# Kernel optimization log

Hardware: AMD Instinct MI355X
Metric: run time of the kernel (lower is better)

Reference implementation:

```python
import jax, jax.numpy as jnp
import numpy as np

B, L, H, NH, P = 4, 1024, 1024, 16, 2048
HD = H // NH


def setup_inputs() -> dict:
    key = jax.random.key(0)
    ks = jax.random.split(key, 6)
    x = jax.random.normal(ks[0], (B, L, H), dtype=jnp.float32)
    # torch.nn.Linear weights are [out, in]
    Wqkv = jax.random.normal(ks[1], (3 * H, H), dtype=jnp.float32) * 0.02
    bqkv = jnp.zeros((3 * H,), dtype=jnp.float32)
    Wo = jax.random.normal(ks[2], (H, H), dtype=jnp.float32) * 0.02
    bo = jnp.zeros((H,), dtype=jnp.float32)
    Er = jax.random.normal(ks[3], (NH, P, HD), dtype=jnp.float32)
    # causal mask: True where attention is disallowed (masked_fill semantics)
    mask = jnp.triu(jnp.ones((L, L), dtype=bool), k=1)
    return {"x": x, "mask": mask, "Wqkv": Wqkv, "bqkv": bqkv,
            "Wo": Wo, "bo": bo, "Er": Er}


def reference(x, mask, Wqkv, bqkv, Wo, bo, Er):
    b, l, d = x.shape
    nh, p, hd = Er.shape
    qkv = x @ Wqkv.T + bqkv                      # [b, l, 3d]
    q, k, v = jnp.split(qkv, 3, axis=-1)
    q = q.reshape(b, l, nh, hd).transpose(0, 2, 1, 3)   # [b, nh, l, hd]
    k = k.reshape(b, l, nh, hd).transpose(0, 2, 1, 3)
    v = v.reshape(b, l, nh, hd).transpose(0, 2, 1, 3)

    scores = jnp.einsum('bnlh,bnkh->bnlk', q, k) / jnp.sqrt(
        jnp.asarray(hd, dtype=x.dtype))

    # relative positions (j - i), torch negative-index wraparound -> mod p
    pos = jnp.arange(l)
    rel = (pos[None, :] - pos[:, None]) % p      # [l, l] in [0, p)
    # Equivalent to einsum('bnlh,rnlkh->bnlk', q, Er[:, rel][None]) but
    # computed as q @ Er^T over all positions then gathered (same math,
    # avoids materializing the [nh, l, l, hd] tensor).
    QEr_full = jnp.einsum('bnlh,nph->bnlp', q, Er)       # [b, nh, l, p]
    i_idx = pos[:, None]                          # broadcasts with rel
    QEr = QEr_full[:, :, i_idx, rel]              # [b, nh, l, l]

    a = scores + QEr
    a = jnp.where(mask, -jnp.inf, a)
    a = jax.nn.softmax(a, axis=-1)                # dropout: eval mode (identity)

    out = jnp.einsum('bnlk,bnkh->bnlh', a, v)     # [b, nh, l, hd]
    out = out.transpose(0, 2, 1, 3).reshape(b, l, d)
    return out @ Wo.T + bo
```

## Files before the change

### kernel.cpp

```cpp
#include <hip/hip_runtime.h>

typedef unsigned short u16;
typedef __bf16 bf16x8 __attribute__((ext_vector_type(8)));
typedef unsigned short u16x8 __attribute__((ext_vector_type(8)));
typedef float f32x4 __attribute__((ext_vector_type(4)));

#define MFMA16(a, b, c) __builtin_amdgcn_mfma_f32_16x16x32_bf16((a), (b), (c), 0, 0, 0)

#define WAVE_LDS_FENCE() do { \
  asm volatile("s_waitcnt lgkmcnt(0)" ::: "memory"); \
  __builtin_amdgcn_sched_barrier(0); \
} while (0)

#define GLDS(gp, lp) __builtin_amdgcn_global_load_lds( \
    (const __attribute__((address_space(1))) unsigned int*)(gp), \
    (__attribute__((address_space(3))) unsigned int*)(lp), 16, 0, 0)

__device__ __forceinline__ u16 f2b(float f) {
  unsigned u = __float_as_uint(f);
  u += 0x7fffu + ((u >> 16) & 1u);
  return (u16)(u >> 16);
}
__device__ __forceinline__ float b2f(u16 h) {
  return __uint_as_float(((unsigned)h) << 16);
}

__global__ void cvt_bf16(const float* __restrict__ src, u16* __restrict__ dst, int n4) {
  int i = blockIdx.x * blockDim.x + threadIdx.x;
  if (i >= n4) return;
  float4 v = *(const float4*)(src + (size_t)i * 4);
  *(ushort4*)(dst + (size_t)i * 4) = make_ushort4(f2b(v.x), f2b(v.y), f2b(v.z), f2b(v.w));
}

__global__ void build_F(const float* __restrict__ Er, u16* __restrict__ Fb) {
  int i = blockIdx.x * blockDim.x + threadIdx.x;
  int base = i * 4;
  int d = base & 63;
  int m = (base >> 6) & 1023;
  int n = base >> 16;
  int sm = (2048 - m) & 2047;
  float4 v = *(const float4*)(Er + ((size_t)(n * 2048 + sm) * 64 + d));
  *(ushort4*)(Fb + (size_t)base) = make_ushort4(f2b(v.x), f2b(v.y), f2b(v.z), f2b(v.w));
}

__global__ __launch_bounds__(256) void transpose_v(const u16* __restrict__ V, u16* __restrict__ Vt) {
  __shared__ u16 T[4096];
  const int bn = blockIdx.x, i0 = blockIdx.y * 64;
  const int t = threadIdx.x;
#pragma unroll
  for (int s = 0; s < 2; ++s) {
    int ch = t + 256 * s;
    int i = ch >> 3, c = ch & 7;
    u16x8 v = *(const u16x8*)&V[(size_t)((bn << 10) + i0 + i) * 64 + c * 8];
#pragma unroll
    for (int e = 0; e < 8; ++e) {
      int d = c * 8 + e;
      T[d * 64 + ((((i >> 3) ^ (d & 7) ^ ((d >> 3) & 7)) & 7) << 3) + (i & 7)] = v[e];
    }
  }
  __syncthreads();
#pragma unroll
  for (int s = 0; s < 2; ++s) {
    int ch = t + 256 * s;
    int d = ch >> 3, cc = ch & 7;
    u16x8 o = *(const u16x8*)&T[d * 64 + (((cc ^ (d & 7) ^ ((d >> 3) & 7)) & 7) << 3)];
    *(u16x8*)&Vt[(size_t)((bn << 6) + d) * 1024 + i0 + cc * 8] = o;
  }
}

__global__ __launch_bounds__(256) void gemm_qkv(const u16* __restrict__ A, const u16* __restrict__ Bw,
                                                const float* __restrict__ bias,
                                                u16* __restrict__ Qo, u16* __restrict__ Ko,
                                                u16* __restrict__ Vo) {
  __shared__ u16 As[8][128][8];
  __shared__ u16 Bs[8][128][8];
  const int m0 = blockIdx.y * 128, n0 = blockIdx.x * 128;
  const int t = threadIdx.x, lane = t & 63, w = t >> 6;
  const int wr = w >> 1, wc = w & 1;
  const int l16 = lane & 15, lg = lane >> 4;
  f32x4 acc[4][4] = {};

  for (int k0 = 0; k0 < 1024; k0 += 64) {
#pragma unroll
    for (int s = 0; s < 4; ++s) {
      int c = t + 256 * s;
      int r = c & 127, g = c >> 7;
      GLDS(&A[(size_t)(m0 + r) * 1024 + k0 + g * 8], &As[g][r][0]);
      GLDS(&Bw[(size_t)(n0 + r) * 1024 + k0 + g * 8], &Bs[g][r][0]);
    }
    __syncthreads();
#pragma unroll
    for (int kk = 0; kk < 2; ++kk) {
      bf16x8 af[4], bfr[4];
#pragma unroll
      for (int m = 0; m < 4; ++m) af[m] = *(const bf16x8*)&As[lg + 4 * kk][wr * 64 + m * 16 + l16][0];
#pragma unroll
      for (int n = 0; n < 4; ++n) bfr[n] = *(const bf16x8*)&Bs[lg + 4 * kk][wc * 64 + n * 16 + l16][0];
#pragma unroll
      for (int m = 0; m < 4; ++m)
#pragma unroll
        for (int n = 0; n < 4; ++n) acc[m][n] = MFMA16(af[m], bfr[n], acc[m][n]);
    }
    __syncthreads();
  }

#pragma unroll
  for (int n = 0; n < 4; ++n) {
    int col = n0 + wc * 64 + n * 16 + l16;
    float bq = bias[col];
    int which = col >> 10;
    int h = col & 1023;
    int head = h >> 6, d = h & 63;
    u16* dst = which == 0 ? Qo : (which == 1 ? Ko : Vo);
    float scale = which == 1 ? 0.125f : 1.0f;
#pragma unroll
    for (int m = 0; m < 4; ++m) {
#pragma unroll
      for (int r = 0; r < 4; ++r) {
        int row = m0 + wr * 64 + m * 16 + lg * 4 + r;
        int b = row >> 10, ii = row & 1023;
        float v = (acc[m][n][r] + bq) * scale;
        dst[(size_t)(((b * 16 + head) << 10) + ii) * 64 + d] = f2b(v);
      }
    }
  }
}

__global__ __launch_bounds__(256) void gemm_out(const u16* __restrict__ A, const u16* __restrict__ Bw,
                                                const float* __restrict__ bias, float* __restrict__ Co) {
  __shared__ u16 As[8][128][8];
  __shared__ u16 Bs[8][128][8];
  const int m0 = blockIdx.y * 128, n0 = blockIdx.x * 128;
  const int t = threadIdx.x, lane = t & 63, w = t >> 6;
  const int wr = w >> 1, wc = w & 1;
  const int l16 = lane & 15, lg = lane >> 4;
  f32x4 acc[4][4] = {};

  for (int k0 = 0; k0 < 1024; k0 += 64) {
#pragma unroll
    for (int s = 0; s < 4; ++s) {
      int c = t + 256 * s;
      int r = c & 127, g = c >> 7;
      GLDS(&A[(size_t)(m0 + r) * 1024 + k0 + g * 8], &As[g][r][0]);
      GLDS(&Bw[(size_t)(n0 + r) * 1024 + k0 + g * 8], &Bs[g][r][0]);
    }
    __syncthreads();
#pragma unroll
    for (int kk = 0; kk < 2; ++kk) {
      bf16x8 af[4], bfr[4];
#pragma unroll
      for (int m = 0; m < 4; ++m) af[m] = *(const bf16x8*)&As[lg + 4 * kk][wr * 64 + m * 16 + l16][0];
#pragma unroll
      for (int n = 0; n < 4; ++n) bfr[n] = *(const bf16x8*)&Bs[lg + 4 * kk][wc * 64 + n * 16 + l16][0];
#pragma unroll
      for (int m = 0; m < 4; ++m)
#pragma unroll
        for (int n = 0; n < 4; ++n) acc[m][n] = MFMA16(af[m], bfr[n], acc[m][n]);
    }
    __syncthreads();
  }

#pragma unroll
  for (int n = 0; n < 4; ++n) {
    int col = n0 + wc * 64 + n * 16 + l16;
    float bq = bias[col];
#pragma unroll
    for (int m = 0; m < 4; ++m) {
#pragma unroll
      for (int r = 0; r < 4; ++r) {
        int row = m0 + wr * 64 + m * 16 + lg * 4 + r;
        Co[(size_t)row * 1024 + col] = acc[m][n][r] + bq;
      }
    }
  }
}

__global__ __launch_bounds__(256) void attn_kernel(const u16* __restrict__ Qg, const u16* __restrict__ Kg,
                                                   const u16* __restrict__ Vtg, const u16* __restrict__ Fg,
                                                   u16* __restrict__ AO) {
  __shared__ u16 Kl[4096];
  __shared__ u16 Vl[4096];
  __shared__ u16 Fl[8192];
  __shared__ u16 Bnd[4][16][84];
  __shared__ u16 Pl[4][1024];

  const int bn = blockIdx.x;
  const int b = bn >> 4, n = bn & 15;
  const int qt = 15 - (int)blockIdx.y;
  const int i0 = qt * 64;
  const int t = threadIdx.x, lane = t & 63, w = t >> 6;
  const int l16 = lane & 15, lg = lane >> 4;

  const int rr0 = t >> 3, cc0 = t & 7;
  const int rr1 = (t + 256) >> 3, cc1 = t & 7;
  const int rr2 = (t + 512) >> 3, cc2 = t & 7;
  const int rr3 = (t + 768) >> 3, cc3 = t & 7;

  bf16x8 qf[2];
  {
    const u16* qp = &Qg[(size_t)((bn << 10) + i0 + (w << 4) + l16) * 64 + lg * 8];
    qf[0] = *(const bf16x8*)qp;
    qf[1] = *(const bf16x8*)(qp + 32);
  }

  float mrun[4], lsum[4];
  f32x4 ao[4] = {};
#pragma unroll
  for (int r = 0; r < 4; ++r) { mrun[r] = -3.0e38f; lsum[r] = 0.0f; }

  u16x8 rk0, rk1, rv0, rv1, rf0, rf1, rf2, rf3;

#define LOAD_STAGE(jt_) do { \
    int j0_ = (jt_) * 64, mb_ = i0 - j0_ - 63; \
    rk0 = *(const u16x8*)&Kg[(size_t)((bn << 10) + j0_ + rr0) * 64 + cc0 * 8]; \
    rk1 = *(const u16x8*)&Kg[(size_t)((bn << 10) + j0_ + rr1) * 64 + cc1 * 8]; \
    rv0 = *(const u16x8*)&Vtg[(size_t)((bn << 6) + rr0) * 1024 + j0_ + cc0 * 8]; \
    rv1 = *(const u16x8*)&Vtg[(size_t)((bn << 6) + rr1) * 1024 + j0_ + cc1 * 8]; \
    int m0_ = mb_ + rr0; m0_ = m0_ < 0 ? 0 : (m0_ > 1023 ? 1023 : m0_); \
    int m1_ = mb_ + rr1; m1_ = m1_ < 0 ? 0 : (m1_ > 1023 ? 1023 : m1_); \
    int m2_ = mb_ + rr2; m2_ = m2_ < 0 ? 0 : (m2_ > 1023 ? 1023 : m2_); \
    int m3_ = mb_ + rr3; m3_ = m3_ < 0 ? 0 : (m3_ > 1023 ? 1023 : m3_); \
    rf0 = *(const u16x8*)&Fg[(size_t)((n << 10) + m0_) * 64 + cc0 * 8]; \
    rf1 = *(const u16x8*)&Fg[(size_t)((n << 10) + m1_) * 64 + cc1 * 8]; \
    rf2 = *(const u16x8*)&Fg[(size_t)((n << 10) + m2_) * 64 + cc2 * 8]; \
    rf3 = *(const u16x8*)&Fg[(size_t)((n << 10) + m3_) * 64 + cc3 * 8]; \
  } while (0)

  LOAD_STAGE(0);

  for (int jt = 0; jt <= qt; ++jt) {
    const bool diag = (jt == qt);

    *(u16x8*)&Kl[rr0 * 64 + (((cc0 ^ (rr0 & 7)) & 7) << 3)] = rk0;
    *(u16x8*)&Kl[rr1 * 64 + (((cc1 ^ (rr1 & 7)) & 7) << 3)] = rk1;
    *(u16x8*)&Vl[rr0 * 64 + (((cc0 ^ (rr0 & 7)) & 7) << 3)] = rv0;
    *(u16x8*)&Vl[rr1 * 64 + (((cc1 ^ (rr1 & 7)) & 7) << 3)] = rv1;
    *(u16x8*)&Fl[rr0 * 64 + (((cc0 ^ (rr0 & 7)) & 7) << 3)] = rf0;
    *(u16x8*)&Fl[rr1 * 64 + (((cc1 ^ (rr1 & 7)) & 7) << 3)] = rf1;
    *(u16x8*)&Fl[rr2 * 64 + (((cc2 ^ (rr2 & 7)) & 7) << 3)] = rf2;
    *(u16x8*)&Fl[rr3 * 64 + (((cc3 ^ (rr3 & 7)) & 7) << 3)] = rf3;
    __syncthreads();

    if (jt < qt) LOAD_STAGE(jt + 1);

    f32x4 sc[4] = {};
#pragma unroll
    for (int kk = 0; kk < 2; ++kk)
#pragma unroll
      for (int nn = 0; nn < 4; ++nn) {
        int jr = nn * 16 + l16;
        bf16x8 kb = *(const bf16x8*)&Kl[jr * 64 + ((((lg + 4 * kk) ^ (jr & 7)) & 7) << 3)];
        sc[nn] = MFMA16(qf[kk], kb, sc[nn]);
      }
    f32x4 bb[5] = {};
#pragma unroll
    for (int kk = 0; kk < 2; ++kk)
#pragma unroll
      for (int ct = 0; ct < 5; ++ct) {
        int trow = (w << 4) + ct * 16 + l16;
        bf16x8 fb = *(const bf16x8*)&Fl[trow * 64 + ((((lg + 4 * kk) ^ (trow & 7)) & 7) << 3)];
        bb[ct] = MFMA16(qf[kk], fb, bb[ct]);
      }
#pragma unroll
    for (int ct = 0; ct < 5; ++ct)
#pragma unroll
      for (int r = 0; r < 4; ++r)
        Bnd[w][lg * 4 + r][ct * 16 + l16] = f2b(bb[ct][r]);
    WAVE_LDS_FENCE();

    const unsigned* bw = (const unsigned*)&Bnd[w][0][0];
    float pv[4][4];
#pragma unroll
    for (int r = 0; r < 4; ++r) {
      int il = lg * 4 + r;
      int c0 = il - l16 + 63;
      int u0 = il * 84 + c0;
      int sh = (u0 & 1) << 4;
      float stmp[4];
      float mx = -3.0e38f;
#pragma unroll
      for (int nn = 0; nn < 4; ++nn) {
        unsigned dv = bw[(u0 >> 1) - 8 * nn];
        float s = sc[nn][r] + b2f((u16)((dv >> sh) & 0xffffu));
        if (diag && (c0 - 16 * nn + (w << 4) < 63)) s = -1.0e30f;
        stmp[nn] = s;
        mx = fmaxf(mx, s);
      }
#pragma unroll
      for (int off = 1; off < 16; off <<= 1) mx = fmaxf(mx, __shfl_xor(mx, off));
      float mnew = fmaxf(mrun[r], mx);
      float scl = __expf(mrun[r] - mnew);
      float rs = 0.0f;
#pragma unroll
      for (int nn = 0; nn < 4; ++nn) {
        pv[nn][r] = __expf(stmp[nn] - mnew);
        rs += pv[nn][r];
      }
      lsum[r] = lsum[r] * scl + rs;
      mrun[r] = mnew;
#pragma unroll
      for (int nd = 0; nd < 4; ++nd) ao[nd][r] *= scl;
    }

#pragma unroll
    for (int nn = 0; nn < 4; ++nn)
#pragma unroll
      for (int r = 0; r < 4; ++r) {
        int i = lg * 4 + r, j = nn * 16 + l16;
        Pl[w][i * 64 + ((((j >> 3) ^ (i & 7)) & 7) << 3) + (j & 7)] = f2b(pv[nn][r]);
      }
    WAVE_LDS_FENCE();
#pragma unroll
    for (int kk = 0; kk < 2; ++kk) {
      bf16x8 pa = *(const bf16x8*)&Pl[w][l16 * 64 + ((((lg + 4 * kk) ^ (l16 & 7)) & 7) << 3)];
#pragma unroll
      for (int nd = 0; nd < 4; ++nd) {
        int dr = nd * 16 + l16;
        bf16x8 vb = *(const bf16x8*)&Vl[dr * 64 + ((((lg + 4 * kk) ^ (dr & 7)) & 7) << 3)];
        ao[nd] = MFMA16(pa, vb, ao[nd]);
      }
    }
    __syncthreads();
  }

#pragma unroll
  for (int r = 0; r < 4; ++r)
#pragma unroll
    for (int off = 1; off < 16; off <<= 1) lsum[r] += __shfl_xor(lsum[r], off);

#pragma unroll
  for (int nd = 0; nd < 4; ++nd)
#pragma unroll
    for (int r = 0; r < 4; ++r) {
      int i = i0 + (w << 4) + lg * 4 + r;
      int d = nd * 16 + l16;
      float v = ao[nd][r] / lsum[r];
      AO[(size_t)((b << 10) + i) * 1024 + n * 64 + d] = f2b(v);
    }
#undef LOAD_STAGE
}

extern "C" void kernel_launch(void* const* d_in, const int* in_sizes, int n_in,
                              void* d_out, int out_size, void* d_ws, size_t ws_size,
                              hipStream_t stream) {
  (void)in_sizes; (void)n_in; (void)out_size; (void)ws_size;
  const float* x    = (const float*)d_in[0];
  const float* Wqkv = (const float*)d_in[2];
  const float* bqkv = (const float*)d_in[3];
  const float* Wo   = (const float*)d_in[4];
  const float* bo   = (const float*)d_in[5];
  const float* Er   = (const float*)d_in[6];
  float* out = (float*)d_out;

  char* p = (char*)d_ws;
  u16* xb    = (u16*)p; p += (size_t)4096 * 1024 * 2;
  u16* wqkvb = (u16*)p; p += (size_t)3072 * 1024 * 2;
  u16* wob   = (u16*)p; p += (size_t)1024 * 1024 * 2;
  u16* Fb    = (u16*)p; p += (size_t)16 * 1024 * 64 * 2;
  u16* Qb    = (u16*)p; p += (size_t)64 * 1024 * 64 * 2;
  u16* Kb    = (u16*)p; p += (size_t)64 * 1024 * 64 * 2;
  u16* Vb    = (u16*)p; p += (size_t)64 * 1024 * 64 * 2;
  u16* Vtb   = (u16*)p; p += (size_t)64 * 1024 * 64 * 2;
  u16* AO    = (u16*)p; p += (size_t)4096 * 1024 * 2;

  cvt_bf16<<<4096, 256, 0, stream>>>(x, xb, 1048576);
  cvt_bf16<<<3072, 256, 0, stream>>>(Wqkv, wqkvb, 786432);
  cvt_bf16<<<1024, 256, 0, stream>>>(Wo, wob, 262144);
  build_F<<<1024, 256, 0, stream>>>(Er, Fb);
  gemm_qkv<<<dim3(24, 32), 256, 0, stream>>>(xb, wqkvb, bqkv, Qb, Kb, Vb);
  transpose_v<<<dim3(64, 16), 256, 0, stream>>>(Vb, Vtb);
  attn_kernel<<<dim3(64, 16), 256, 0, stream>>>(Qb, Kb, Vtb, Fb, AO);
  gemm_out<<<dim3(8, 32), 256, 0, stream>>>(AO, wob, bo, out);
}
```

Before: 174.5 us.

## Double-buffer LDS in projection GEMMs and merge fp32-to-bf16 conversion launches

Both projection GEMMs now use two 32-wide K-slices of LDS and prefetch the next slice with global_load_lds while MFMAs run on the current one. A single vmcnt wait plus barrier per step replaces the two __syncthreads, so global load latency overlaps with compute. The three conversion kernels are merged into one launch to cut launch overhead. In exchange each step has a smaller K slice and a barrier every 32 K elements, and correctness depends on the vmcnt wait covering the LDS-direct loads.

```diff
diff --git a/kernel.cpp b/kernel.cpp
--- a/kernel.cpp
+++ b/kernel.cpp
@@ -12,6 +12,12 @@
   __builtin_amdgcn_sched_barrier(0); \
 } while (0)
 
+#define PHASE_BARRIER() do { \
+  asm volatile("s_waitcnt vmcnt(0)" ::: "memory"); \
+  __builtin_amdgcn_sched_barrier(0); \
+  __builtin_amdgcn_s_barrier(); \
+} while (0)
+
 #define GLDS(gp, lp) __builtin_amdgcn_global_load_lds( \
     (const __attribute__((address_space(1))) unsigned int*)(gp), \
     (__attribute__((address_space(3))) unsigned int*)(lp), 16, 0, 0)
@@ -25,11 +31,16 @@
   return __uint_as_float(((unsigned)h) << 16);
 }
 
-__global__ void cvt_bf16(const float* __restrict__ src, u16* __restrict__ dst, int n4) {
+__global__ void cvt_all(const float* __restrict__ x, u16* __restrict__ xb,
+                        const float* __restrict__ w1, u16* __restrict__ w1b,
+                        const float* __restrict__ w2, u16* __restrict__ w2b) {
   int i = blockIdx.x * blockDim.x + threadIdx.x;
-  if (i >= n4) return;
-  float4 v = *(const float4*)(src + (size_t)i * 4);
-  *(ushort4*)(dst + (size_t)i * 4) = make_ushort4(f2b(v.x), f2b(v.y), f2b(v.z), f2b(v.w));
+  const float* s; u16* d; int off;
+  if (i < 1048576)      { s = x;  d = xb;  off = i; }
+  else if (i < 1835008) { s = w1; d = w1b; off = i - 1048576; }
+  else                  { s = w2; d = w2b; off = i - 1835008; }
+  float4 v = *(const float4*)(s + (size_t)off * 4);
+  *(ushort4*)(d + (size_t)off * 4) = make_ushort4(f2b(v.x), f2b(v.y), f2b(v.z), f2b(v.w));
 }
 
 __global__ void build_F(const float* __restrict__ Er, u16* __restrict__ Fb) {
@@ -72,37 +83,43 @@
                                                 const float* __restrict__ bias,
                                                 u16* __restrict__ Qo, u16* __restrict__ Ko,
                                                 u16* __restrict__ Vo) {
-  __shared__ u16 As[8][128][8];
-  __shared__ u16 Bs[8][128][8];
+  __shared__ u16 As[2][4][128][8];
+  __shared__ u16 Bs[2][4][128][8];
   const int m0 = blockIdx.y * 128, n0 = blockIdx.x * 128;
   const int t = threadIdx.x, lane = t & 63, w = t >> 6;
   const int wr = w >> 1, wc = w & 1;
   const int l16 = lane & 15, lg = lane >> 4;
   f32x4 acc[4][4] = {};
-
-  for (int k0 = 0; k0 < 1024; k0 += 64) {
-#pragma unroll
-    for (int s = 0; s < 4; ++s) {
-      int c = t + 256 * s;
-      int r = c & 127, g = c >> 7;
-      GLDS(&A[(size_t)(m0 + r) * 1024 + k0 + g * 8], &As[g][r][0]);
-      GLDS(&Bw[(size_t)(n0 + r) * 1024 + k0 + g * 8], &Bs[g][r][0]);
-    }
-    __syncthreads();
-#pragma unroll
-    for (int kk = 0; kk < 2; ++kk) {
-      bf16x8 af[4], bfr[4];
-#pragma unroll
-      for (int m = 0; m < 4; ++m) af[m] = *(const bf16x8*)&As[lg + 4 * kk][wr * 64 + m * 16 + l16][0];
-#pragma unroll
-      for (int n = 0; n < 4; ++n) bfr[n] = *(const bf16x8*)&Bs[lg + 4 * kk][wc * 64 + n * 16 + l16][0];
-#pragma unroll
-      for (int m = 0; m < 4; ++m)
-#pragma unroll
-        for (int n = 0; n < 4; ++n) acc[m][n] = MFMA16(af[m], bfr[n], acc[m][n]);
-    }
-    __syncthreads();
-  }
+  const int c0 = t, r0 = c0 & 127, g0 = c0 >> 7;
+  const int c1 = t + 256, r1 = c1 & 127, g1 = c1 >> 7;
+
+#define STAGE(buf, k0) do { \
+    GLDS(&A[(size_t)(m0 + r0) * 1024 + (k0) + g0 * 8], &As[buf][g0][r0][0]); \
+    GLDS(&A[(size_t)(m0 + r1) * 1024 + (k0) + g1 * 8], &As[buf][g1][r1][0]); \
+    GLDS(&Bw[(size_t)(n0 + r0) * 1024 + (k0) + g0 * 8], &Bs[buf][g0][r0][0]); \
+    GLDS(&Bw[(size_t)(n0 + r1) * 1024 + (k0) + g1 * 8], &Bs[buf][g1][r1][0]); \
+  } while (0)
+
+  STAGE(0, 0);
+  PHASE_BARRIER();
+
+#pragma unroll 2
+  for (int kt = 0; kt < 32; ++kt) {
+    const int buf = kt & 1;
+    if (kt < 31) STAGE(buf ^ 1, (kt + 1) * 32);
+    __builtin_amdgcn_sched_barrier(0);
+    bf16x8 af[4], bfr[4];
+#pragma unroll
+    for (int m = 0; m < 4; ++m) af[m] = *(const bf16x8*)&As[buf][lg][wr * 64 + m * 16 + l16][0];
+#pragma unroll
+    for (int n = 0; n < 4; ++n) bfr[n] = *(const bf16x8*)&Bs[buf][lg][wc * 64 + n * 16 + l16][0];
+#pragma unroll
+    for (int m = 0; m < 4; ++m)
+#pragma unroll
+      for (int n = 0; n < 4; ++n) acc[m][n] = MFMA16(af[m], bfr[n], acc[m][n]);
+    PHASE_BARRIER();
+  }
+#undef STAGE
 
 #pragma unroll
   for (int n = 0; n < 4; ++n) {
@@ -128,37 +145,43 @@
 
 __global__ __launch_bounds__(256) void gemm_out(const u16* __restrict__ A, const u16* __restrict__ Bw,
                                                 const float* __restrict__ bias, float* __restrict__ Co) {
-  __shared__ u16 As[8][128][8];
-  __shared__ u16 Bs[8][128][8];
+  __shared__ u16 As[2][4][128][8];
+  __shared__ u16 Bs[2][4][128][8];
   const int m0 = blockIdx.y * 128, n0 = blockIdx.x * 128;
   const int t = threadIdx.x, lane = t & 63, w = t >> 6;
   const int wr = w >> 1, wc = w & 1;
   const int l16 = lane & 15, lg = lane >> 4;
   f32x4 acc[4][4] = {};
-
-  for (int k0 = 0; k0 < 1024; k0 += 64) {
-#pragma unroll
-    for (int s = 0; s < 4; ++s) {
-      int c = t + 256 * s;
-      int r = c & 127, g = c >> 7;
-      GLDS(&A[(size_t)(m0 + r) * 1024 + k0 + g * 8], &As[g][r][0]);
-      GLDS(&Bw[(size_t)(n0 + r) * 1024 + k0 + g * 8], &Bs[g][r][0]);
-    }
-    __syncthreads();
-#pragma unroll
-    for (int kk = 0; kk < 2; ++kk) {
-      bf16x8 af[4], bfr[4];
-#pragma unroll
-      for (int m = 0; m < 4; ++m) af[m] = *(const bf16x8*)&As[lg + 4 * kk][wr * 64 + m * 16 + l16][0];
-#pragma unroll
-      for (int n = 0; n < 4; ++n) bfr[n] = *(const bf16x8*)&Bs[lg + 4 * kk][wc * 64 + n * 16 + l16][0];
-#pragma unroll
-      for (int m = 0; m < 4; ++m)
-#pragma unroll
-        for (int n = 0; n < 4; ++n) acc[m][n] = MFMA16(af[m], bfr[n], acc[m][n]);
-    }
-    __syncthreads();
-  }
+  const int c0 = t, r0 = c0 & 127, g0 = c0 >> 7;
+  const int c1 = t + 256, r1 = c1 & 127, g1 = c1 >> 7;
+
+#define STAGE(buf, k0) do { \
+    GLDS(&A[(size_t)(m0 + r0) * 1024 + (k0) + g0 * 8], &As[buf][g0][r0][0]); \
+    GLDS(&A[(size_t)(m0 + r1) * 1024 + (k0) + g1 * 8], &As[buf][g1][r1][0]); \
+    GLDS(&Bw[(size_t)(n0 + r0) * 1024 + (k0) + g0 * 8], &Bs[buf][g0][r0][0]); \
+    GLDS(&Bw[(size_t)(n0 + r1) * 1024 + (k0) + g1 * 8], &Bs[buf][g1][r1][0]); \
+  } while (0)
+
+  STAGE(0, 0);
+  PHASE_BARRIER();
+
+#pragma unroll 2
+  for (int kt = 0; kt < 32; ++kt) {
+    const int buf = kt & 1;
+    if (kt < 31) STAGE(buf ^ 1, (kt + 1) * 32);
+    __builtin_amdgcn_sched_barrier(0);
+    bf16x8 af[4], bfr[4];
+#pragma unroll
+    for (int m = 0; m < 4; ++m) af[m] = *(const bf16x8*)&As[buf][lg][wr * 64 + m * 16 + l16][0];
+#pragma unroll
+    for (int n = 0; n < 4; ++n) bfr[n] = *(const bf16x8*)&Bs[buf][lg][wc * 64 + n * 16 + l16][0];
+#pragma unroll
+    for (int m = 0; m < 4; ++m)
+#pragma unroll
+      for (int n = 0; n < 4; ++n) acc[m][n] = MFMA16(af[m], bfr[n], acc[m][n]);
+    PHASE_BARRIER();
+  }
+#undef STAGE
 
 #pragma unroll
   for (int n = 0; n < 4; ++n) {
@@ -363,9 +386,7 @@
   u16* Vtb   = (u16*)p; p += (size_t)64 * 1024 * 64 * 2;
   u16* AO    = (u16*)p; p += (size_t)4096 * 1024 * 2;
 
-  cvt_bf16<<<4096, 256, 0, stream>>>(x, xb, 1048576);
-  cvt_bf16<<<3072, 256, 0, stream>>>(Wqkv, wqkvb, 786432);
-  cvt_bf16<<<1024, 256, 0, stream>>>(Wo, wob, 262144);
+  cvt_all<<<8192, 256, 0, stream>>>(x, xb, Wqkv, wqkvb, Wo, wob);
   build_F<<<1024, 256, 0, stream>>>(Er, Fb);
   gemm_qkv<<<dim3(24, 32), 256, 0, stream>>>(xb, wqkvb, bqkv, Qb, Kb, Vb);
   transpose_v<<<dim3(64, 16), 256, 0, stream>>>(Vb, Vtb);
```

Result: faster. 166.2 us (-4.8%).
